# Performance work log

Measured on AMD Instinct MI355X. Metric: run time of the kernel, lower is better.

The kernel has to match this reference:

```python
import jax, jax.numpy as jnp
import numpy as np

N = 50000       # nodes
E = 800000      # edges (before self-loops)
NFEAT = 256
NHID = 16       # per-head hidden dim
HEADS = 8
NCLASS = 16
NEG_SLOPE = 0.2  # PyG GATConv default leaky-relu slope


def setup_inputs() -> dict:
    key = jax.random.key(0)
    ks = jax.random.split(key, 10)
    s = 0.05  # weight scale for numerical sanity
    return {
        "x": jax.random.normal(ks[0], (N, NFEAT), jnp.float32),
        "edge_index": jax.random.randint(ks[1], (2, E), 0, N, dtype=jnp.int32),
        "W1": jax.random.normal(ks[2], (NFEAT, HEADS * NHID), jnp.float32) * s,
        "att_src1": jax.random.normal(ks[3], (HEADS, NHID), jnp.float32) * s,
        "att_dst1": jax.random.normal(ks[4], (HEADS, NHID), jnp.float32) * s,
        "b1": jnp.zeros((HEADS * NHID,), jnp.float32),
        "W2": jax.random.normal(ks[5], (HEADS * NHID, NCLASS), jnp.float32) * s,
        "att_src2": jax.random.normal(ks[6], (1, NCLASS), jnp.float32) * s,
        "att_dst2": jax.random.normal(ks[7], (1, NCLASS), jnp.float32) * s,
        "b2": jnp.zeros((NCLASS,), jnp.float32),
    }


def gat_conv(x, edge_index, W, a_src, a_dst, b, heads, out_c, concat):
    """Faithful PyG GATConv (eval mode: dropout off, add_self_loops=True)."""
    n = x.shape[0]
    loop = jnp.arange(n, dtype=edge_index.dtype)
    src = jnp.concatenate([edge_index[0], loop])  # [E+N]
    dst = jnp.concatenate([edge_index[1], loop])  # [E+N]
    h = (x @ W).reshape(n, heads, out_c)          # [N, H, C]
    # per-node attention logits
    alpha_src = jnp.einsum('nhc,hc->nh', h, a_src)  # [N, H]
    alpha_dst = jnp.einsum('nhc,hc->nh', h, a_dst)  # [N, H]
    e = jax.nn.leaky_relu(alpha_src[src] + alpha_dst[dst], NEG_SLOPE)  # [E+N, H]
    # segment softmax over incoming edges of each dst node (self-loop guarantees nonempty)
    m = jax.lax.stop_gradient(jax.ops.segment_max(e, dst, num_segments=n))
    p = jnp.exp(e - m[dst])
    denom = jax.ops.segment_sum(p, dst, num_segments=n)
    a = p / denom[dst]                              # [E+N, H]
    out = jax.ops.segment_sum(a[:, :, None] * h[src], dst, num_segments=n)  # [N, H, C]
    out = out.reshape(n, heads * out_c) if concat else out.mean(axis=1)
    return out + b


def reference(x, edge_index, W1, att_src1, att_dst1, b1, W2, att_src2, att_dst2, b2):
    h1 = jax.nn.elu(gat_conv(x, edge_index, W1, att_src1, att_dst1, b1, HEADS, NHID, True))
    return gat_conv(h1, edge_index, W2, att_src2, att_dst2, b2, 1, NCLASS, False)
```

## Files before the change

kernel.cpp:

```cpp
#include <hip/hip_runtime.h>
#include <hip/hip_bf16.h>

#define NNODES 50000
#define NEDGES 800000
#define NFEATS 256
#define NHID 16
#define HEADS 8
#define NCLS 16
#define NEG_SLOPE 0.2f
#define TOTE (NEDGES + NNODES)
#define RSTRIDE 64
#define NBUCK 196
#define NPB 256
#define BCAP 4864
#define S1_EPT 16
#define BIN_BLOCKS ((TOTE + 4095) / 4096)
#define GSTRIDE 16

typedef __attribute__((ext_vector_type(8))) short short8;
typedef __attribute__((ext_vector_type(4))) float floatx4;

static __device__ __forceinline__ short f2bf(float f) {
    __hip_bfloat16 b = __float2bfloat16(f);
    return *reinterpret_cast<short*>(&b);
}

#define AS1 __attribute__((address_space(1)))
#define AS3 __attribute__((address_space(3)))

static __device__ __forceinline__ void ld_lds16(const void* g, void* l) {
#if __has_builtin(__builtin_amdgcn_global_load_lds)
    __builtin_amdgcn_global_load_lds((const AS1 void*)g, (AS3 void*)l, 16, 0, 0);
#endif
}


__global__ __launch_bounds__(256) void k_bin(const int* __restrict__ ei,
                                             int* __restrict__ gcnt, int* __restrict__ barr,
                                             const float* __restrict__ W,
                                             const float* __restrict__ a_s,
                                             const float* __restrict__ a_d,
                                             short* __restrict__ Wsw) {
    int tid = threadIdx.x;
    if (blockIdx.x >= BIN_BLOCKS) {
        int t = (blockIdx.x - BIN_BLOCKS) * 256 + tid;
        if (t >= 4608) return;
        short8 b;
        if (t < 4096) {
            int kc = t >> 9, nt = (t >> 6) & 7, lane = t & 63;
            int quad = lane >> 4, lo = lane & 15;
#pragma unroll
            for (int j = 0; j < 8; j++)
                b[j] = f2bf(W[(size_t)(kc * 32 + quad * 8 + j) * 128 + nt * 16 + lo]);
        } else {
            int t2 = t - 4096;
            int kc = t2 >> 6, lane = t2 & 63;
            int quad = lane >> 4, lo = lane & 15;
            int h = lo & 7;
            const float* av = (lo < 8) ? (a_s + h * 16) : (a_d + h * 16);
#pragma unroll
            for (int j = 0; j < 8; j++) {
                int k = kc * 32 + quad * 8 + j;
                float acc = 0.f;
#pragma unroll
                for (int c = 0; c < 16; c++) acc += W[(size_t)k * 128 + h * 16 + c] * av[c];
                b[j] = f2bf(acc);
            }
        }
        *(short8*)(Wsw + (size_t)t * 8) = b;
        return;
    }

    __shared__ int lcnt[NBUCK], lbase[NBUCK];
    if (tid < NBUCK) lcnt[tid] = 0;
    __syncthreads();
    int e0 = blockIdx.x * (256 * S1_EPT) + tid;
    int s[S1_EPT], d[S1_EPT], rk[S1_EPT];
#pragma unroll
    for (int k = 0; k < S1_EPT; k++) {
        int e = e0 + k * 256;
        bool v = e < TOTE;
        int ss = 0, dd = 0;
        if (v) {
            if (e < NEDGES) { ss = ei[e]; dd = ei[NEDGES + e]; }
            else            { ss = e - NEDGES; dd = ss; }
        }
        s[k] = ss; d[k] = dd;
        rk[k] = v ? atomicAdd(&lcnt[dd >> 8], 1) : -1;
    }
    __syncthreads();
    if (tid < NBUCK) lbase[tid] = lcnt[tid] ? atomicAdd(&gcnt[tid * GSTRIDE], lcnt[tid]) : 0;
    __syncthreads();
#pragma unroll
    for (int k = 0; k < S1_EPT; k++) {
        if (rk[k] >= 0) {
            int b = d[k] >> 8;
            int pos = lbase[b] + rk[k];
            if (pos < BCAP)
                barr[(size_t)b * BCAP + pos] = ((d[k] & 255) << 16) | s[k];
        }
    }
}


__global__ __launch_bounds__(256) void k_csr(const int* __restrict__ gcnt,
                                             const int* __restrict__ barr,
                                             int* __restrict__ cnt, int* __restrict__ csr) {
    __shared__ int lcnt[NPB];
    __shared__ unsigned short lcsr[NPB * 65];
    int b = blockIdx.x, tid = threadIdx.x;
    lcnt[tid] = 0;
    __syncthreads();
    int n = min(gcnt[b * GSTRIDE], BCAP);
    int nodeBase = b << 8;
    for (int i = tid; i < n; i += 256) {
        int e = barr[(size_t)b * BCAP + i];
        int ln = e >> 16;
        int r = atomicAdd(&lcnt[ln], 1);
        if (r < RSTRIDE) lcsr[ln * 65 + r] = (unsigned short)(e & 0xFFFF);
    }
    __syncthreads();
    int node = nodeBase + tid;
    if (node < NNODES) cnt[node] = min(lcnt[tid], RSTRIDE);
    for (int i = tid; i < NPB * RSTRIDE; i += 256) {
        int ln = i >> 6;
        int nn = nodeBase + ln;
        if (nn < NNODES && (i & 63) < min(lcnt[ln], RSTRIDE))
            csr[(size_t)nodeBase * RSTRIDE + i] = (int)lcsr[ln * 65 + (i & 63)];
    }
}


__global__ __launch_bounds__(256) void k_gemm1(const float* __restrict__ x,
                                               const short* __restrict__ Wsw,
                                               __hip_bfloat16* __restrict__ h1,
                                               float* __restrict__ as1, float* __restrict__ ad1) {
    __shared__ short bsw[32768];
    int tid  = threadIdx.x;
    int wave = tid >> 6;
    int lane = tid & 63;
    int quad = lane >> 4;
    int lo   = lane & 15;

#if __has_builtin(__builtin_amdgcn_global_load_lds)
    {
        const char* gsrc = (const char*)Wsw + (size_t)wave * 1024 + (size_t)lane * 16;
        char* ldst = (char*)bsw + wave * 1024;
#pragma unroll
        for (int it = 0; it < 16; it++)
            ld_lds16(gsrc + it * 4096, ldst + it * 4096);
    }
#else
    {
        const uint4* g4 = (const uint4*)Wsw;
        uint4* l4 = (uint4*)bsw;
#pragma unroll
        for (int it = 0; it < 16; it++) l4[it * 256 + tid] = g4[it * 256 + tid];
    }
#endif
    short8 wafr[8];
#pragma unroll
    for (int kc = 0; kc < 8; kc++)
        wafr[kc] = *(const short8*)(Wsw + (size_t)(4096 + kc * 64 + lane) * 8);
    __syncthreads();

    int rowBase = blockIdx.x * 128 + wave * 32;
    const float* xa[2];
#pragma unroll
    for (int mt = 0; mt < 2; mt++) {
        int row = rowBase + mt * 16 + lo;
        row = (row < NNODES) ? row : (NNODES - 1);
        xa[mt] = x + (size_t)row * 256 + quad * 8;
    }

    floatx4 acc[2][8], accA[2];
#pragma unroll
    for (int mt = 0; mt < 2; mt++) {
        accA[mt] = (floatx4){0.f, 0.f, 0.f, 0.f};
#pragma unroll
        for (int nt = 0; nt < 8; nt++) acc[mt][nt] = (floatx4){0.f, 0.f, 0.f, 0.f};
    }

    float4 a0[2], a1[2];
#pragma unroll
    for (int mt = 0; mt < 2; mt++) {
        a0[mt] = *(const float4*)(xa[mt]);
        a1[mt] = *(const float4*)(xa[mt] + 4);
    }

    for (int kc = 0; kc < 8; kc++) {
        float4 n0[2], n1[2];
        if (kc < 7) {
#pragma unroll
            for (int mt = 0; mt < 2; mt++) {
                n0[mt] = *(const float4*)(xa[mt] + (kc + 1) * 32);
                n1[mt] = *(const float4*)(xa[mt] + (kc + 1) * 32 + 4);
            }
        }
        short8 afr[2];
#pragma unroll
        for (int mt = 0; mt < 2; mt++) {
            union { short8 s; __hip_bfloat162 h[4]; } u;
            u.h[0] = __float22bfloat162_rn(make_float2(a0[mt].x, a0[mt].y));
            u.h[1] = __float22bfloat162_rn(make_float2(a0[mt].z, a0[mt].w));
            u.h[2] = __float22bfloat162_rn(make_float2(a1[mt].x, a1[mt].y));
            u.h[3] = __float22bfloat162_rn(make_float2(a1[mt].z, a1[mt].w));
            afr[mt] = u.s;
        }
#pragma unroll
        for (int nt = 0; nt < 8; nt++) {
            short8 bfr = *(const short8*)&bsw[((kc * 8 + nt) * 64 + lane) * 8];
            acc[0][nt] = __builtin_amdgcn_mfma_f32_16x16x32_bf16(afr[0], bfr, acc[0][nt], 0, 0, 0);
            acc[1][nt] = __builtin_amdgcn_mfma_f32_16x16x32_bf16(afr[1], bfr, acc[1][nt], 0, 0, 0);
        }
        accA[0] = __builtin_amdgcn_mfma_f32_16x16x32_bf16(afr[0], wafr[kc], accA[0], 0, 0, 0);
        accA[1] = __builtin_amdgcn_mfma_f32_16x16x32_bf16(afr[1], wafr[kc], accA[1], 0, 0, 0);
#pragma unroll
        for (int mt = 0; mt < 2; mt++) { a0[mt] = n0[mt]; a1[mt] = n1[mt]; }
    }

#pragma unroll
    for (int mt = 0; mt < 2; mt++)
#pragma unroll
        for (int nt = 0; nt < 8; nt++)
#pragma unroll
            for (int reg = 0; reg < 4; reg++) {
                int row = rowBase + mt * 16 + quad * 4 + reg;
                int col = nt * 16 + lo;
                if (row < NNODES)
                    h1[(size_t)row * 128 + col] = __float2bfloat16(acc[mt][nt][reg]);
            }
#pragma unroll
    for (int mt = 0; mt < 2; mt++)
#pragma unroll
        for (int reg = 0; reg < 4; reg++) {
            int row = rowBase + mt * 16 + quad * 4 + reg;
            if (row < NNODES) {
                float v = accA[mt][reg];
                if (lo < 8) as1[(size_t)row * 8 + lo] = v;
                else        ad1[(size_t)row * 8 + (lo - 8)] = v;
            }
        }
}


__global__ __launch_bounds__(256) void k_agg1(const int* __restrict__ cnt, const int* __restrict__ csr,
                                              const __hip_bfloat16* __restrict__ h1,
                                              const float* __restrict__ as1, const float* __restrict__ ad1,
                                              const float* __restrict__ b1, __hip_bfloat16* __restrict__ h1act) {
    int wid  = blockIdx.x * 4 + (threadIdx.x >> 6);
    int lane = threadIdx.x & 63;
    int cl   = lane & 15;
    int node = wid * 4 + (lane >> 4);
    int deg  = min(cnt[node], RSTRIDE);
    int head = cl >> 1;
    float adst = ad1[node * 8 + head];
    int rs = node * RSTRIDE;
    int rowv[4];
#pragma unroll
    for (int r = 0; r < 4; r++) rowv[r] = csr[rs + cl + 16 * r];
    int md = deg;
    md = max(md, __shfl_xor(md, 16));
    md = max(md, __shfl_xor(md, 32));

    float acc[8] = {0.f, 0.f, 0.f, 0.f, 0.f, 0.f, 0.f, 0.f};
    float s = 0.f;
#pragma unroll
    for (int r = 0; r < 4; r++) {
        int rbase = r << 4;
        if (rbase >= md) break;
        int lim = min(16, md - rbase);
        for (int i2 = 0; i2 < lim; i2 += 4) {
            float p[4];
            union { short8 v; __hip_bfloat162 h[4]; } u[4];
#pragma unroll
            for (int t = 0; t < 4; t++) {
                int idx = rbase + i2 + t;
                int src = __shfl(rowv[r], (lane & 48) | ((i2 + t) & 15));
                p[t] = 0.f;
                u[t].v = (short8){0, 0, 0, 0, 0, 0, 0, 0};
                if (idx < deg) {
                    u[t].v = *(const short8*)(h1 + (size_t)src * 128 + cl * 8);
                    float e = as1[src * 8 + head] + adst;
                    e = (e > 0.f) ? e : NEG_SLOPE * e;
                    p[t] = __expf(e);
                }
            }
            s += (p[0] + p[1]) + (p[2] + p[3]);
#pragma unroll
            for (int t = 0; t < 4; t++)
#pragma unroll
                for (int q = 0; q < 4; q++) {
                    float2 f = __bfloat1622float2(u[t].h[q]);
                    acc[q * 2]     = fmaf(p[t], f.x, acc[q * 2]);
                    acc[q * 2 + 1] = fmaf(p[t], f.y, acc[q * 2 + 1]);
                }
        }
    }
    float is = 1.f / s;
    union { short8 v; short us[8]; } pk;
#pragma unroll
    for (int q = 0; q < 8; q++) {
        float v = acc[q] * is + b1[cl * 8 + q];
        v = (v > 0.f) ? v : (__expf(v) - 1.f);
        pk.us[q] = f2bf(v);
    }
    *(short8*)(h1act + (size_t)node * 128 + cl * 8) = pk.v;
}


__global__ __launch_bounds__(256) void k_gemm2(const __hip_bfloat16* __restrict__ h1act,
                                               const float* __restrict__ W2,
                                               const float* __restrict__ a_src,
                                               const float* __restrict__ a_dst,
                                               float* __restrict__ h2,
                                               float* __restrict__ as2, float* __restrict__ ad2) {
    __shared__ float w[128 * 16];
    __shared__ float hr[16][129];
    int tid = threadIdx.x;
    int row0 = blockIdx.x * 16;
    for (int i = tid; i < 2048; i += 256) w[i] = W2[i];
    {
        int r = tid >> 4, k8 = (tid & 15) * 8;
        int gr = row0 + r;
        union { short8 v; __hip_bfloat162 h[4]; } u;
        if (gr < NNODES) u.v = *(const short8*)(h1act + (size_t)gr * 128 + k8);
        else             u.v = (short8){0, 0, 0, 0, 0, 0, 0, 0};
#pragma unroll
        for (int q = 0; q < 4; q++) {
            float2 f = __bfloat1622float2(u.h[q]);
            hr[r][k8 + q * 2]     = f.x;
            hr[r][k8 + q * 2 + 1] = f.y;
        }
    }
    __syncthreads();
    int r = tid >> 4, c = tid & 15;
    float acc = 0.f;
#pragma unroll 8
    for (int k = 0; k < 128; k++) acc += hr[r][k] * w[k * 16 + c];
    int gr = row0 + r;
    if (gr < NNODES) h2[(size_t)gr * 16 + c] = acc;
    float sv = acc * a_src[c];
    float dv = acc * a_dst[c];
#pragma unroll
    for (int o = 1; o <= 8; o <<= 1) {
        sv += __shfl_xor(sv, o);
        dv += __shfl_xor(dv, o);
    }
    if (c == 0 && gr < NNODES) { as2[gr] = sv; ad2[gr] = dv; }
}


__global__ __launch_bounds__(256) void k_agg2(const int* __restrict__ cnt, const int* __restrict__ csr,
                                              const float* __restrict__ h2, const float* __restrict__ as2,
                                              const float* __restrict__ ad2, const float* __restrict__ b2,
                                              float* __restrict__ out) {
    int wid  = blockIdx.x * 4 + (threadIdx.x >> 6);
    int lane = threadIdx.x & 63;
    int sub  = lane & 15;
    int slot = sub >> 2;
    int c4   = sub & 3;
    int node = wid * 4 + (lane >> 4);
    int deg  = min(cnt[node], RSTRIDE);
    float adst = ad2[node];
    int rs = node * RSTRIDE;
    int rowv[4];
#pragma unroll
    for (int r = 0; r < 4; r++) rowv[r] = csr[rs + sub + 16 * r];
    int md = deg;
    md = max(md, __shfl_xor(md, 16));
    md = max(md, __shfl_xor(md, 32));

    float4 acc = make_float4(0.f, 0.f, 0.f, 0.f);
    float s = 0.f;
#pragma unroll
    for (int r = 0; r < 4; r++) {
        int rbase = r << 4;
        if (rbase >= md) break;
        int lim = min(16, md - rbase);
        for (int i2 = 0; i2 < lim; i2 += 8) {
            int ia = rbase + i2 + slot;
            int ib = ia + 4;
            int sa = __shfl(rowv[r], (lane & 48) | ((i2 + slot) & 15));
            int sb = __shfl(rowv[r], (lane & 48) | ((i2 + 4 + slot) & 15));
            float p0 = 0.f, p1 = 0.f;
            float4 r0 = make_float4(0.f, 0.f, 0.f, 0.f);
            float4 r1 = make_float4(0.f, 0.f, 0.f, 0.f);
            if (ia < deg) {
                r0 = *(const float4*)(h2 + (size_t)sa * 16 + c4 * 4);
                float e = as2[sa] + adst;
                e = (e > 0.f) ? e : NEG_SLOPE * e;
                p0 = __expf(e);
            }
            if (ib < deg) {
                r1 = *(const float4*)(h2 + (size_t)sb * 16 + c4 * 4);
                float e = as2[sb] + adst;
                e = (e > 0.f) ? e : NEG_SLOPE * e;
                p1 = __expf(e);
            }
            s += p0 + p1;
            acc.x = fmaf(p0, r0.x, fmaf(p1, r1.x, acc.x));
            acc.y = fmaf(p0, r0.y, fmaf(p1, r1.y, acc.y));
            acc.z = fmaf(p0, r0.z, fmaf(p1, r1.z, acc.z));
            acc.w = fmaf(p0, r0.w, fmaf(p1, r1.w, acc.w));
        }
    }
#pragma unroll
    for (int o = 4; o <= 8; o <<= 1) {
        acc.x += __shfl_xor(acc.x, o);
        acc.y += __shfl_xor(acc.y, o);
        acc.z += __shfl_xor(acc.z, o);
        acc.w += __shfl_xor(acc.w, o);
        s += __shfl_xor(s, o);
    }
    if (slot == 0) {
        float is = 1.f / s;
        float4 o4;
        o4.x = acc.x * is + b2[c4 * 4 + 0];
        o4.y = acc.y * is + b2[c4 * 4 + 1];
        o4.z = acc.z * is + b2[c4 * 4 + 2];
        o4.w = acc.w * is + b2[c4 * 4 + 3];
        *(float4*)(out + (size_t)node * 16 + c4 * 4) = o4;
    }
}


extern "C" void kernel_launch(void* const* d_in, const int* in_sizes, int n_in,
                              void* d_out, int out_size, void* d_ws, size_t ws_size,
                              hipStream_t stream) {
    const float* x    = (const float*)d_in[0];
    const int*   ei   = (const int*)d_in[1];
    const float* W1   = (const float*)d_in[2];
    const float* a_s1 = (const float*)d_in[3];
    const float* a_d1 = (const float*)d_in[4];
    const float* b1   = (const float*)d_in[5];
    const float* W2   = (const float*)d_in[6];
    const float* a_s2 = (const float*)d_in[7];
    const float* a_d2 = (const float*)d_in[8];
    const float* b2   = (const float*)d_in[9];
    float* out = (float*)d_out;

    char* p = (char*)d_ws;
    auto alloc = [&](size_t bytes) -> char* {
        char* q = p;
        p += (bytes + 255) & ~(size_t)255;
        return q;
    };
    int*  gcnt = (int*)alloc((size_t)NBUCK * GSTRIDE * 4);
    int*  barr = (int*)alloc((size_t)NBUCK * BCAP * 4);
    int*  cnt  = (int*)alloc((size_t)NNODES * 4);
    int*  csr  = (int*)alloc((size_t)NNODES * RSTRIDE * 4);
    short* Wsw = (short*)alloc((size_t)36864 * 2);
    __hip_bfloat16* h1 = (__hip_bfloat16*)alloc((size_t)NNODES * 128 * 2);
    float* as1 = (float*)alloc((size_t)NNODES * 8 * 4);
    float* ad1 = (float*)alloc((size_t)NNODES * 8 * 4);
    __hip_bfloat16* h1act = (__hip_bfloat16*)alloc((size_t)NNODES * 128 * 2);
    float* h2  = (float*)as1;
    float* as2 = (float*)barr;
    float* ad2 = (float*)barr + NNODES;

    hipMemsetAsync(gcnt, 0, (size_t)NBUCK * GSTRIDE * 4, stream);
    hipLaunchKernelGGL(k_bin,   dim3(BIN_BLOCKS + 18), dim3(256), 0, stream,
                       ei, gcnt, barr, W1, a_s1, a_d1, Wsw);
    hipLaunchKernelGGL(k_csr,   dim3(NBUCK), dim3(256), 0, stream, gcnt, barr, cnt, csr);
    hipLaunchKernelGGL(k_gemm1, dim3((NNODES + 127) / 128), dim3(256), 0, stream, x, Wsw, h1, as1, ad1);
    hipLaunchKernelGGL(k_agg1,  dim3(NNODES / 16), dim3(256), 0, stream, cnt, csr, h1, as1, ad1, b1, h1act);
    hipLaunchKernelGGL(k_gemm2, dim3((NNODES + 15) / 16), dim3(256), 0, stream, h1act, W2, a_s2, a_d2, h2, as2, ad2);
    hipLaunchKernelGGL(k_agg2,  dim3(NNODES / 16), dim3(256), 0, stream, cnt, csr, h2, as2, ad2, b2, out);
}
```

Baseline: 216.0 us.

## Assign one wavefront per node in aggregation kernels with cross-slot reduction

Both aggregation kernels now map a whole 64-lane wavefront to a single destination node instead of four nodes per wave. Lanes split that node's incoming edges into parallel slots, and partial sums are combined with xor shuffles at the end. This removes the divergence from mixing node degrees within one wave and puts more loads in flight per node. In exchange it launches four times as many blocks, adds a reduction, and leaves many lanes idle for low-degree nodes.

```diff
diff --git a/kernel.cpp b/kernel.cpp
--- a/kernel.cpp
+++ b/kernel.cpp
@@ -248,64 +248,67 @@
                                               const __hip_bfloat16* __restrict__ h1,
                                               const float* __restrict__ as1, const float* __restrict__ ad1,
                                               const float* __restrict__ b1, __hip_bfloat16* __restrict__ h1act) {
-    int wid  = blockIdx.x * 4 + (threadIdx.x >> 6);
+    int node = blockIdx.x * 4 + (threadIdx.x >> 6);
     int lane = threadIdx.x & 63;
     int cl   = lane & 15;
-    int node = wid * 4 + (lane >> 4);
+    int slot = lane >> 4;
+    int head = cl >> 1;
     int deg  = min(cnt[node], RSTRIDE);
-    int head = cl >> 1;
     float adst = ad1[node * 8 + head];
-    int rs = node * RSTRIDE;
-    int rowv[4];
-#pragma unroll
-    for (int r = 0; r < 4; r++) rowv[r] = csr[rs + cl + 16 * r];
-    int md = deg;
-    md = max(md, __shfl_xor(md, 16));
-    md = max(md, __shfl_xor(md, 32));
+    int rowv = csr[node * RSTRIDE + lane];
 
     float acc[8] = {0.f, 0.f, 0.f, 0.f, 0.f, 0.f, 0.f, 0.f};
     float s = 0.f;
-#pragma unroll
-    for (int r = 0; r < 4; r++) {
-        int rbase = r << 4;
-        if (rbase >= md) break;
-        int lim = min(16, md - rbase);
-        for (int i2 = 0; i2 < lim; i2 += 4) {
-            float p[4];
-            union { short8 v; __hip_bfloat162 h[4]; } u[4];
-#pragma unroll
-            for (int t = 0; t < 4; t++) {
-                int idx = rbase + i2 + t;
-                int src = __shfl(rowv[r], (lane & 48) | ((i2 + t) & 15));
-                p[t] = 0.f;
-                u[t].v = (short8){0, 0, 0, 0, 0, 0, 0, 0};
-                if (idx < deg) {
-                    u[t].v = *(const short8*)(h1 + (size_t)src * 128 + cl * 8);
-                    float e = as1[src * 8 + head] + adst;
-                    e = (e > 0.f) ? e : NEG_SLOPE * e;
-                    p[t] = __expf(e);
-                }
-            }
-            s += (p[0] + p[1]) + (p[2] + p[3]);
-#pragma unroll
-            for (int t = 0; t < 4; t++)
-#pragma unroll
-                for (int q = 0; q < 4; q++) {
-                    float2 f = __bfloat1622float2(u[t].h[q]);
-                    acc[q * 2]     = fmaf(p[t], f.x, acc[q * 2]);
-                    acc[q * 2 + 1] = fmaf(p[t], f.y, acc[q * 2 + 1]);
-                }
-        }
-    }
-    float is = 1.f / s;
-    union { short8 v; short us[8]; } pk;
+    for (int i2 = 0; i2 < deg; i2 += 8) {
+        int ia = i2 + slot;
+        int ib = ia + 4;
+        int sa = __shfl(rowv, ia & 63);
+        int sb = __shfl(rowv, ib & 63);
+        union { short8 v; __hip_bfloat162 h[4]; } ua, ub;
+        float pa = 0.f, pb = 0.f;
+        ua.v = (short8){0, 0, 0, 0, 0, 0, 0, 0};
+        ub.v = (short8){0, 0, 0, 0, 0, 0, 0, 0};
+        if (ia < deg) {
+            ua.v = *(const short8*)(h1 + (size_t)sa * 128 + cl * 8);
+            float e = as1[sa * 8 + head] + adst;
+            e = (e > 0.f) ? e : NEG_SLOPE * e;
+            pa = __expf(e);
+        }
+        if (ib < deg) {
+            ub.v = *(const short8*)(h1 + (size_t)sb * 128 + cl * 8);
+            float e = as1[sb * 8 + head] + adst;
+            e = (e > 0.f) ? e : NEG_SLOPE * e;
+            pb = __expf(e);
+        }
+        s += pa + pb;
+#pragma unroll
+        for (int q = 0; q < 4; q++) {
+            float2 fa = __bfloat1622float2(ua.h[q]);
+            float2 fb = __bfloat1622float2(ub.h[q]);
+            acc[q * 2]     = fmaf(pa, fa.x, acc[q * 2]);
+            acc[q * 2 + 1] = fmaf(pa, fa.y, acc[q * 2 + 1]);
+            acc[q * 2]     = fmaf(pb, fb.x, acc[q * 2]);
+            acc[q * 2 + 1] = fmaf(pb, fb.y, acc[q * 2 + 1]);
+        }
+    }
 #pragma unroll
     for (int q = 0; q < 8; q++) {
-        float v = acc[q] * is + b1[cl * 8 + q];
-        v = (v > 0.f) ? v : (__expf(v) - 1.f);
-        pk.us[q] = f2bf(v);
-    }
-    *(short8*)(h1act + (size_t)node * 128 + cl * 8) = pk.v;
+        acc[q] += __shfl_xor(acc[q], 16);
+        acc[q] += __shfl_xor(acc[q], 32);
+    }
+    s += __shfl_xor(s, 16);
+    s += __shfl_xor(s, 32);
+    if (slot == 0) {
+        float is = 1.f / s;
+        union { short8 v; short us[8]; } pk;
+#pragma unroll
+        for (int q = 0; q < 8; q++) {
+            float v = acc[q] * is + b1[cl * 8 + q];
+            v = (v > 0.f) ? v : (__expf(v) - 1.f);
+            pk.us[q] = f2bf(v);
+        }
+        *(short8*)(h1act + (size_t)node * 128 + cl * 8) = pk.v;
+    }
 }
 
 
@@ -355,58 +358,35 @@
                                               const float* __restrict__ h2, const float* __restrict__ as2,
                                               const float* __restrict__ ad2, const float* __restrict__ b2,
                                               float* __restrict__ out) {
-    int wid  = blockIdx.x * 4 + (threadIdx.x >> 6);
+    int node = blockIdx.x * 4 + (threadIdx.x >> 6);
     int lane = threadIdx.x & 63;
-    int sub  = lane & 15;
-    int slot = sub >> 2;
-    int c4   = sub & 3;
-    int node = wid * 4 + (lane >> 4);
+    int c4   = lane & 3;
+    int slot = lane >> 2;
     int deg  = min(cnt[node], RSTRIDE);
     float adst = ad2[node];
-    int rs = node * RSTRIDE;
-    int rowv[4];
-#pragma unroll
-    for (int r = 0; r < 4; r++) rowv[r] = csr[rs + sub + 16 * r];
-    int md = deg;
-    md = max(md, __shfl_xor(md, 16));
-    md = max(md, __shfl_xor(md, 32));
+    int rowv = csr[node * RSTRIDE + lane];
 
     float4 acc = make_float4(0.f, 0.f, 0.f, 0.f);
     float s = 0.f;
-#pragma unroll
-    for (int r = 0; r < 4; r++) {
-        int rbase = r << 4;
-        if (rbase >= md) break;
-        int lim = min(16, md - rbase);
-        for (int i2 = 0; i2 < lim; i2 += 8) {
-            int ia = rbase + i2 + slot;
-            int ib = ia + 4;
-            int sa = __shfl(rowv[r], (lane & 48) | ((i2 + slot) & 15));
-            int sb = __shfl(rowv[r], (lane & 48) | ((i2 + 4 + slot) & 15));
-            float p0 = 0.f, p1 = 0.f;
-            float4 r0 = make_float4(0.f, 0.f, 0.f, 0.f);
-            float4 r1 = make_float4(0.f, 0.f, 0.f, 0.f);
-            if (ia < deg) {
-                r0 = *(const float4*)(h2 + (size_t)sa * 16 + c4 * 4);
-                float e = as2[sa] + adst;
-                e = (e > 0.f) ? e : NEG_SLOPE * e;
-                p0 = __expf(e);
-            }
-            if (ib < deg) {
-                r1 = *(const float4*)(h2 + (size_t)sb * 16 + c4 * 4);
-                float e = as2[sb] + adst;
-                e = (e > 0.f) ? e : NEG_SLOPE * e;
-                p1 = __expf(e);
-            }
-            s += p0 + p1;
-            acc.x = fmaf(p0, r0.x, fmaf(p1, r1.x, acc.x));
-            acc.y = fmaf(p0, r0.y, fmaf(p1, r1.y, acc.y));
-            acc.z = fmaf(p0, r0.z, fmaf(p1, r1.z, acc.z));
-            acc.w = fmaf(p0, r0.w, fmaf(p1, r1.w, acc.w));
-        }
-    }
-#pragma unroll
-    for (int o = 4; o <= 8; o <<= 1) {
+    for (int i2 = 0; i2 < deg; i2 += 16) {
+        int ia = i2 + slot;
+        int sa = __shfl(rowv, ia & 63);
+        float p0 = 0.f;
+        float4 r0 = make_float4(0.f, 0.f, 0.f, 0.f);
+        if (ia < deg) {
+            r0 = *(const float4*)(h2 + (size_t)sa * 16 + c4 * 4);
+            float e = as2[sa] + adst;
+            e = (e > 0.f) ? e : NEG_SLOPE * e;
+            p0 = __expf(e);
+        }
+        s += p0;
+        acc.x = fmaf(p0, r0.x, acc.x);
+        acc.y = fmaf(p0, r0.y, acc.y);
+        acc.z = fmaf(p0, r0.z, acc.z);
+        acc.w = fmaf(p0, r0.w, acc.w);
+    }
+#pragma unroll
+    for (int o = 4; o <= 32; o <<= 1) {
         acc.x += __shfl_xor(acc.x, o);
         acc.y += __shfl_xor(acc.y, o);
         acc.z += __shfl_xor(acc.z, o);
@@ -464,7 +444,7 @@
                        ei, gcnt, barr, W1, a_s1, a_d1, Wsw);
     hipLaunchKernelGGL(k_csr,   dim3(NBUCK), dim3(256), 0, stream, gcnt, barr, cnt, csr);
     hipLaunchKernelGGL(k_gemm1, dim3((NNODES + 127) / 128), dim3(256), 0, stream, x, Wsw, h1, as1, ad1);
-    hipLaunchKernelGGL(k_agg1,  dim3(NNODES / 16), dim3(256), 0, stream, cnt, csr, h1, as1, ad1, b1, h1act);
+    hipLaunchKernelGGL(k_agg1,  dim3(NNODES / 4), dim3(256), 0, stream, cnt, csr, h1, as1, ad1, b1, h1act);
     hipLaunchKernelGGL(k_gemm2, dim3((NNODES + 15) / 16), dim3(256), 0, stream, h1act, W2, a_s2, a_d2, h2, as2, ad2);
-    hipLaunchKernelGGL(k_agg2,  dim3(NNODES / 16), dim3(256), 0, stream, cnt, csr, h2, as2, ad2, b2, out);
-}
+    hipLaunchKernelGGL(k_agg2,  dim3(NNODES / 4), dim3(256), 0, stream, cnt, csr, h2, as2, ad2, b2, out);
+}
```

Result: slower. 221.4 us (+2.5%).
